# Optimization experiments

Measured on AMD Instinct MI355X. Metric: run time of the kernel, lower is better.

Reference implementation:

```python
import jax, jax.numpy as jnp
import numpy as np

TEMPERATURE = 0.07
UNIFORMITY_THRESHOLD = 0.1
SEPARATION_MARGIN = 2.0
W_SUPCON = 1.0
W_SEPARATION = 0.5
W_UNIFORMITY = 0.5
NUM_MASKS = 6


def setup_inputs() -> dict:
    key = jax.random.key(0)
    k1, k2, k3 = jax.random.split(key, 3)
    B, H, Wd, D = 16, 33, 33, 512
    emb = jax.random.normal(k1, (B, H, Wd, D), dtype=jnp.float32)
    emb = emb / jnp.linalg.norm(emb, axis=-1, keepdims=True)  # module expects normalized embeddings
    masks = jax.random.uniform(k2, (B, NUM_MASKS, H, Wd), dtype=jnp.float32)
    is_forged = jax.random.uniform(k3, (B,), dtype=jnp.float32)
    return {"embeddings": emb, "masks": masks, "is_forged": is_forged}


def _labels(masks):
    # masks: (M, H, W). Channel i writes label i+1 where mask>0.5 (if channel has any mass);
    # later channels overwrite earlier -> equivalent to max over active hits.
    active = masks.sum(axis=(1, 2)) > 0  # (M,)
    hit = (masks > 0.5) & active[:, None, None]
    ids = jnp.arange(1, masks.shape[0] + 1)[:, None, None]
    return jnp.max(jnp.where(hit, ids, 0), axis=0).reshape(-1)  # (H*W,)


def _per_image(emb, masks, forged):
    H, W, D = emb.shape
    feat = emb.reshape(-1, D)  # (N, D)
    N = feat.shape[0]
    labels = _labels(masks)  # (N,) in 0..M
    L = masks.shape[0] + 1  # possible labels 0..6
    onehot = (labels[:, None] == jnp.arange(L)[None, :]).astype(feat.dtype)  # (N, L)
    cnt = onehot.sum(axis=0)  # (L,)
    sums = onehot.T @ feat  # (L, D) per-label sums
    mean_l = sums / jnp.maximum(cnt, 1.0)[:, None]  # safe per-label centroids

    # ---- SupCon (PixelSupConLoss) ----
    logits = (feat @ feat.T) / TEMPERATURE  # (N, N)
    logits = logits - jax.lax.stop_gradient(logits.max(axis=1, keepdims=True))
    same = (labels[:, None] == labels[None, :]).astype(feat.dtype)
    logits_mask = 1.0 - jnp.eye(N, dtype=feat.dtype)
    pos = same * logits_mask
    exp_l = jnp.exp(logits) * logits_mask
    log_prob = logits - jnp.log(exp_l.sum(axis=1, keepdims=True) + 1e-6)
    pos_sum = pos.sum(axis=1)
    mean_lp = (pos * log_prob).sum(axis=1) / jnp.where(pos_sum == 0, 1.0, pos_sum)
    anchor_valid = (pos_sum > 0).astype(feat.dtype)
    n_anchor = anchor_valid.sum()
    supcon = (-mean_lp * anchor_valid).sum() / jnp.maximum(n_anchor, 1.0)
    supcon_valid = n_anchor > 0

    # ---- Inter-instance separation ----
    present = cnt > 0
    cn = (mean_l ** 2).sum(axis=1)  # (L,)
    sq = cn[:, None] + cn[None, :] - 2.0 * (mean_l @ mean_l.T)  # squared centroid dists
    tri = jnp.triu(jnp.ones((L, L), dtype=bool), k=1)
    pair_valid = tri & present[:, None] & present[None, :]
    d = jnp.sqrt(jnp.where(pair_valid, jnp.maximum(sq, 0.0), 1.0))
    terms = jnp.where(pair_valid, jax.nn.relu(SEPARATION_MARGIN - d), 0.0)
    n_pairs = pair_valid.sum().astype(feat.dtype)
    sep = terms.sum() / jnp.maximum(n_pairs, 1.0)
    sep_valid = present.sum() >= 2

    # ---- Uniformity ----
    rn2 = (feat ** 2).sum(axis=1)  # (N,)
    q_l = onehot.T @ rn2  # (L,) per-label sum of squared norms
    var_l = q_l / jnp.maximum(cnt, 1.0) - (mean_l ** 2).sum(axis=1)  # E||e||^2 - ||mean||^2
    lbl_valid = (cnt >= 2) & (var_l > UNIFORMITY_THRESHOLD)
    inst_loss = jnp.where(lbl_valid, var_l - UNIFORMITY_THRESHOLD, 0.0).sum()
    n_lbl = lbl_valid.sum().astype(feat.dtype)
    uni_forged = inst_loss / jnp.maximum(n_lbl, 1.0)
    uni_forged_valid = n_lbl > 0
    mean_all = feat.mean(axis=0)
    var_all = ((feat - mean_all) ** 2).sum(axis=1).mean()
    uni_unf = jnp.where(var_all > UNIFORMITY_THRESHOLD, var_all - UNIFORMITY_THRESHOLD, 0.0)
    uni_unf_valid = var_all > UNIFORMITY_THRESHOLD

    is_f = forged >= 0.5
    uni = jnp.where(is_f, uni_forged, uni_unf)
    uni_valid = jnp.where(is_f, uni_forged_valid, uni_unf_valid)
    return supcon, supcon_valid, sep, sep_valid, uni, uni_valid


def _agg(vals, valids):
    v = valids.astype(vals.dtype)
    n = v.sum()
    return jnp.where(n > 0, (vals * v).sum() / jnp.maximum(n, 1.0), 0.0)


def reference(embeddings, masks, is_forged):
    sc, scv, sp, spv, un, unv = jax.vmap(_per_image)(embeddings, masks, is_forged)
    supcon = _agg(sc, scv)
    separation = _agg(sp, spv)
    uniformity = _agg(un, unv)
    return W_SUPCON * supcon + W_SEPARATION * separation + W_UNIFORMITY * uniformity
```

## Files before the change

kernel.cpp:

```cpp
#include <hip/hip_runtime.h>
#include <math.h>

#define NPIX 1089
#define DIM 512
#define NIMG 16
#define NLBL 8
#define NMASK 6
#define INVT 14.2857142857142857f

#define NGRP 72
#define NROWPAD 1152
#define NT9 9



typedef short v8s __attribute__((ext_vector_type(8)));
typedef float v4f __attribute__((ext_vector_type(4)));

__device__ __forceinline__ float wave_reduce(float x) {
#pragma unroll
  for (int o = 32; o > 0; o >>= 1) x += __shfl_xor(x, o, 64);
  return x;
}
__device__ __forceinline__ unsigned bfbits(float x) {
  unsigned u = __float_as_uint(x);
  return (u + 0x7FFFu + ((u >> 16) & 1u)) >> 16;
}
__device__ __forceinline__ unsigned pk(float lo, float hi) {
  return bfbits(lo) | (bfbits(hi) << 16);
}

__global__ void k_labels(const float* __restrict__ masks, int* __restrict__ labels,
                         float* __restrict__ cnt) {
  int b = blockIdx.x, tid = threadIdx.x;
  int lane = tid & 63, w = tid >> 6;
  __shared__ float msum[NMASK];
  __shared__ float red[4][NLBL];
  if (tid < NMASK) msum[tid] = 0.f;
  __syncthreads();
  float acc[NMASK] = {0.f, 0.f, 0.f, 0.f, 0.f, 0.f};
  for (int p = tid; p < NPIX; p += 256) {
#pragma unroll
    for (int c = 0; c < NMASK; c++) acc[c] += masks[((size_t)b * NMASK + c) * NPIX + p];
  }
#pragma unroll
  for (int c = 0; c < NMASK; c++) {
    float v = wave_reduce(acc[c]);
    if (lane == 0) atomicAdd(&msum[c], v);
  }
  __syncthreads();
  float c8[NLBL] = {0.f, 0.f, 0.f, 0.f, 0.f, 0.f, 0.f, 0.f};
  for (int p = tid; p < NPIX; p += 256) {
    int lab = 0;
#pragma unroll
    for (int c = 0; c < NMASK; c++) {
      float mv = masks[((size_t)b * NMASK + c) * NPIX + p];
      if (mv > 0.5f && msum[c] > 0.f) lab = c + 1;
    }
    labels[b * NPIX + p] = lab;
#pragma unroll
    for (int l = 0; l < NLBL; l++) c8[l] += (lab == l) ? 1.f : 0.f;
  }
#pragma unroll
  for (int l = 0; l < NLBL; l++) c8[l] = wave_reduce(c8[l]);
  if (lane == 0) {
#pragma unroll
    for (int l = 0; l < NLBL; l++) red[w][l] = c8[l];
  }
  __syncthreads();
  if (tid < NLBL)
    cnt[b * NLBL + tid] = red[0][tid] + red[1][tid] + red[2][tid] + red[3][tid];
}

__global__ __launch_bounds__(512) void k_packsum(const float* __restrict__ emb,
                                                 const int* __restrict__ labels,
                                                 uint2* __restrict__ bfemb2,
                                                 float* __restrict__ sums9) {
  int b = blockIdx.y;
  int g9 = blockIdx.x >> 1, dh = blockIdx.x & 1;
  int tid = threadIdx.x, dd = tid & 63, w4 = tid >> 6;
  __shared__ int slab[128];
  __shared__ float4 red[8 * 8 * 64];
  if (tid < 128) {
    int r = g9 * 128 + tid;
    slab[tid] = (r < NPIX) ? labels[b * NPIX + r] : 7;
  }
  __syncthreads();
  float4 fa0 = {0,0,0,0}, fa1 = {0,0,0,0}, fa2 = {0,0,0,0}, fa3 = {0,0,0,0};
  float4 fa4 = {0,0,0,0}, fa5 = {0,0,0,0}, fa6 = {0,0,0,0}, fa7 = {0,0,0,0};
  int kc = dh * 8 + (dd >> 3), q = (dd >> 1) & 3, half = dd & 1;
#pragma unroll
  for (int k = 0; k < 16; k++) {
    int r = g9 * 128 + w4 + k * 8;
    bool v = r < NPIX;
    int rc = v ? r : (NPIX - 1);
    float4 x = ((const float4*)(emb + (size_t)(b * NPIX + rc) * DIM))[dh * 64 + dd];
    if (!v) x = make_float4(0.f, 0.f, 0.f, 0.f);
    uint2 o = make_uint2(pk(x.x, x.y), pk(x.z, x.w));
    bfemb2[((((size_t)(b * NGRP + (r >> 4)) * 16 + kc) * 64) + q * 16 + (r & 15)) * 2 + half] = o;
    int lab = __builtin_amdgcn_readfirstlane(slab[r - g9 * 128]);
    switch (lab) {
      case 0: fa0.x += x.x; fa0.y += x.y; fa0.z += x.z; fa0.w += x.w; break;
      case 1: fa1.x += x.x; fa1.y += x.y; fa1.z += x.z; fa1.w += x.w; break;
      case 2: fa2.x += x.x; fa2.y += x.y; fa2.z += x.z; fa2.w += x.w; break;
      case 3: fa3.x += x.x; fa3.y += x.y; fa3.z += x.z; fa3.w += x.w; break;
      case 4: fa4.x += x.x; fa4.y += x.y; fa4.z += x.z; fa4.w += x.w; break;
      case 5: fa5.x += x.x; fa5.y += x.y; fa5.z += x.z; fa5.w += x.w; break;
      case 6: fa6.x += x.x; fa6.y += x.y; fa6.z += x.z; fa6.w += x.w; break;
      default: fa7.x += x.x; fa7.y += x.y; fa7.z += x.z; fa7.w += x.w; break;
    }
  }
  red[(0 * 8 + w4) * 64 + dd] = fa0; red[(1 * 8 + w4) * 64 + dd] = fa1;
  red[(2 * 8 + w4) * 64 + dd] = fa2; red[(3 * 8 + w4) * 64 + dd] = fa3;
  red[(4 * 8 + w4) * 64 + dd] = fa4; red[(5 * 8 + w4) * 64 + dd] = fa5;
  red[(6 * 8 + w4) * 64 + dd] = fa6; red[(7 * 8 + w4) * 64 + dd] = fa7;
  __syncthreads();
  int l = tid >> 6, d2 = tid & 63;
  float4 s = {0,0,0,0};
#pragma unroll
  for (int ww = 0; ww < 8; ww++) {
    float4 t = red[(l * 8 + ww) * 64 + d2];
    s.x += t.x; s.y += t.y; s.z += t.z; s.w += t.w;
  }
  *(float4*)&sums9[(((size_t)(b * NT9 + g9) * NLBL + l) * DIM) + dh * 256 + d2 * 4] = s;
}

__global__ __launch_bounds__(256) void k_epass3(const uint4* __restrict__ bfemb4,
                                                float* __restrict__ E18) {
  int n = blockIdx.x;
  int img = ((n & 7) << 1) | ((n >> 3) & 1);
  int t = n >> 4;
  int it = 0, rem = t;
  while (rem >= NT9 - it) { rem -= NT9 - it; it++; }
  int jt = it + rem;
  int i0 = it * 128, j0 = jt * 128;
  bool diag = (it == jt);
  int tid = threadIdx.x, lane = tid & 63, w = tid >> 6;
  int wm = w >> 1, wn = w & 1;
  int quad = lane >> 4, l15 = lane & 15;

  size_t uA[4], uB[4];
#pragma unroll
  for (int f = 0; f < 4; f++) {
    uA[f] = ((size_t)(img * NGRP + it * 8 + wm * 4 + f) * 16) * 64 + lane;
    uB[f] = ((size_t)(img * NGRP + jt * 8 + wn * 4 + f) * 16) * 64 + lane;
  }

  v4f acc[4][4];
#pragma unroll
  for (int mf = 0; mf < 4; mf++)
#pragma unroll
    for (int nf = 0; nf < 4; nf++) acc[mf][nf] = (v4f){0.f, 0.f, 0.f, 0.f};

  v8s a0[4], b0[4], a1[4], b1[4];
#define LOADG(kc, AR, BR)                                               \
  {                                                                     \
    _Pragma("unroll") for (int f = 0; f < 4; f++)                       \
        AR[f] = *(const v8s*)(bfemb4 + uA[f] + (kc) * 64);              \
    _Pragma("unroll") for (int f = 0; f < 4; f++)                       \
        BR[f] = *(const v8s*)(bfemb4 + uB[f] + (kc) * 64);              \
  }
#define MFMAG(AR, BR)                                                   \
  {                                                                     \
    _Pragma("unroll") for (int mf = 0; mf < 4; mf++)                    \
        _Pragma("unroll") for (int nf = 0; nf < 4; nf++)                \
            acc[mf][nf] = __builtin_amdgcn_mfma_f32_16x16x32_bf16(      \
                AR[mf], BR[nf], acc[mf][nf], 0, 0, 0);                  \
  }

  LOADG(0, a0, b0);
#pragma unroll
  for (int kc = 0; kc < 16; kc += 2) {
    if (kc + 1 < 16) LOADG(kc + 1, a1, b1);
    MFMAG(a0, b0);
    if (kc + 2 < 16) LOADG(kc + 2, a0, b0);
    MFMAG(a1, b1);
  }
#undef LOADG
#undef MFMAG

  float* Erow = E18 + ((size_t)img * 18 + jt * 2 + wn) * NROWPAD;
  float* Ecol = E18 + ((size_t)img * 18 + it * 2 + wm) * NROWPAD;
  float scol[4] = {0.f, 0.f, 0.f, 0.f};
#pragma unroll
  for (int mf = 0; mf < 4; mf++) {
#pragma unroll
    for (int rr = 0; rr < 4; rr++) {
      int i = i0 + wm * 64 + mf * 16 + quad * 4 + rr;
      float srow = 0.f;
#pragma unroll
      for (int nf = 0; nf < 4; nf++) {
        int j = j0 + wn * 64 + nf * 16 + l15;
        float e = __expf((acc[mf][nf][rr] - 1.f) * INVT);
        bool ok = (j < NPIX) && (!diag || (i != j && i < NPIX));
        e = ok ? e : 0.f;
        srow += e;
        scol[nf] += e;
      }
      srow += __shfl_xor(srow, 1); srow += __shfl_xor(srow, 2);
      srow += __shfl_xor(srow, 4); srow += __shfl_xor(srow, 8);
      if (l15 == 0) Erow[i] = srow;
    }
  }
  if (!diag) {
#pragma unroll
    for (int nf = 0; nf < 4; nf++) {
      float s = scol[nf];
      s += __shfl_xor(s, 16); s += __shfl_xor(s, 32);
      int j = j0 + wn * 64 + nf * 16 + l15;
      if (quad == 0) Ecol[j] = s;
    }
  }
}

__global__ void k_img(const float* __restrict__ sums9, const int* __restrict__ labels,
                      const float* __restrict__ cnt, const float* __restrict__ E18,
                      const float* __restrict__ is_forged, float* __restrict__ per_img) {
  int b = blockIdx.x, tid = threadIdx.x;
  int wave = tid >> 6, lane = tid & 63;
  __shared__ float ssum[NLBL * DIM];
  __shared__ float sCnt[NLBL], sR[NLBL][NLBL];
  __shared__ float sLog, sNA;
  if (tid < NLBL) sCnt[tid] = cnt[b * NLBL + tid];
  if (tid == 0) { sLog = 0.f; sNA = 0.f; }
  for (int o = tid; o < NLBL * DIM; o += 256) {
    float s = 0.f;
#pragma unroll
    for (int g = 0; g < NT9; g++) s += sums9[((size_t)(b * NT9 + g) * NLBL * DIM) + o];
    ssum[o] = s;
  }
  __syncthreads();
  float ll = 0.f, na = 0.f;
  for (int p = tid; p < NPIX; p += 256) {
    int lab = labels[b * NPIX + p];
    if (sCnt[lab] >= 1.5f) {
      float e = 0.f;
#pragma unroll
      for (int s = 0; s < 18; s++) e += E18[((size_t)b * 18 + s) * NROWPAD + p];
      ll += logf(e + 1e-6f);
      na += 1.f;
    }
  }
  ll = wave_reduce(ll); na = wave_reduce(na);
  if (lane == 0) { atomicAdd(&sLog, ll); atomicAdd(&sNA, na); }
  for (int t = wave; t < 36; t += 4) {
    int a = 0, tt = t;
    while (tt >= NLBL - a) { tt -= NLBL - a; a++; }
    int bb = a + tt;
    float d0 = 0.f;
    for (int k = lane; k < DIM; k += 64) d0 += ssum[a * DIM + k] * ssum[bb * DIM + k];
    d0 = wave_reduce(d0);
    if (lane == 0) sR[a][bb] = d0;
  }
  __syncthreads();
  if (tid == 0) {
    float spos = 0.f;
    for (int l = 0; l < NLBL; l++) {
      float c = sCnt[l];
      if (c >= 1.5f) spos += (sR[l][l] - c) * INVT / (c - 1.f) - c * INVT;
    }
    float nA = sNA;
    float sc = nA > 0.f ? (sLog - spos) / nA : 0.f;
    float scv = nA > 0.f ? 1.f : 0.f;
    float inv[NLBL]; int present[NLBL]; int nPres = 0;
    for (int l = 0; l < NLBL; l++) {
      present[l] = sCnt[l] > 0.f;
      nPres += present[l];
      inv[l] = 1.f / fmaxf(sCnt[l], 1.f);
    }
    float sepsum = 0.f; int npairs = 0;
    for (int a = 0; a < NLBL; a++)
      for (int c = a + 1; c < NLBL; c++)
        if (present[a] && present[c]) {
          float sq_ = sR[a][a] * inv[a] * inv[a] + sR[c][c] * inv[c] * inv[c]
                    - 2.f * sR[a][c] * inv[a] * inv[c];
          float dd = sqrtf(fmaxf(sq_, 0.f));
          sepsum += fmaxf(2.f - dd, 0.f);
          npairs++;
        }
    float sep = npairs > 0 ? sepsum / (float)npairs : 0.f;
    float sepv = nPres >= 2 ? 1.f : 0.f;
    float inst = 0.f; int nlbl = 0;
    for (int l = 0; l < NLBL; l++) {
      float var = 1.f - sR[l][l] * inv[l] * inv[l];
      if (sCnt[l] >= 2.f && var > 0.1f) { inst += var - 0.1f; nlbl++; }
    }
    float unif = nlbl > 0 ? inst / (float)nlbl : 0.f;
    float unifv = nlbl > 0 ? 1.f : 0.f;
    float tot2 = 0.f;
    for (int a = 0; a < NLBL; a++) {
      tot2 += sR[a][a];
      for (int c = a + 1; c < NLBL; c++) tot2 += 2.f * sR[a][c];
    }
    float Nf = (float)NPIX;
    float var_all = 1.f - tot2 / (Nf * Nf);
    float uniu = var_all > 0.1f ? var_all - 0.1f : 0.f;
    float uniuv = var_all > 0.1f ? 1.f : 0.f;
    bool isf = is_forged[b] >= 0.5f;
    per_img[b * 6 + 0] = sc;
    per_img[b * 6 + 1] = scv;
    per_img[b * 6 + 2] = sep;
    per_img[b * 6 + 3] = sepv;
    per_img[b * 6 + 4] = isf ? unif : uniu;
    per_img[b * 6 + 5] = isf ? unifv : uniuv;
  }
}

__global__ void k_final(const float* __restrict__ per_img, float* __restrict__ out) {
  if (threadIdx.x == 0) {
    float accv[3] = {0.f, 0.f, 0.f}, accn[3] = {0.f, 0.f, 0.f};
    for (int b = 0; b < NIMG; b++)
      for (int m = 0; m < 3; m++) {
        float v = per_img[b * 6 + m * 2], val = per_img[b * 6 + m * 2 + 1];
        accv[m] += v * val; accn[m] += val;
      }
    float sc = accn[0] > 0.f ? accv[0] / accn[0] : 0.f;
    float sep = accn[1] > 0.f ? accv[1] / accn[1] : 0.f;
    float uni = accn[2] > 0.f ? accv[2] / accn[2] : 0.f;
    out[0] = 1.0f * sc + 0.5f * sep + 0.5f * uni;
  }
}

extern "C" void kernel_launch(void* const* d_in, const int* in_sizes, int n_in,
                              void* d_out, int out_size, void* d_ws, size_t ws_size,
                              hipStream_t stream) {
  const float* emb = (const float*)d_in[0];
  const float* masks = (const float*)d_in[1];
  const float* isf = (const float*)d_in[2];
  float* out = (float*)d_out;
  char* ws = (char*)d_ws;
  size_t off = 0;
  uint4* bfemb4 = (uint4*)(ws + off);
  off += (size_t)NIMG * NGRP * 16 * 64 * 16;
  float* E18 = (float*)(ws + off);    off += sizeof(float) * NIMG * 18 * NROWPAD;
  float* sums9 = (float*)(ws + off);  off += sizeof(float) * NIMG * NT9 * NLBL * DIM;
  int* labels = (int*)(ws + off);     off += sizeof(int) * NIMG * NPIX;
  float* cnt = (float*)(ws + off);    off += sizeof(float) * NIMG * NLBL;
  float* per_img = (float*)(ws + off); off += sizeof(float) * NIMG * 6;

  k_labels<<<NIMG, 256, 0, stream>>>(masks, labels, cnt);
  k_packsum<<<dim3(18, NIMG), 512, 0, stream>>>(emb, labels, (uint2*)bfemb4, sums9);
  k_epass3<<<45 * NIMG, 256, 0, stream>>>(bfemb4, E18);
  k_img<<<NIMG, 256, 0, stream>>>(sums9, labels, cnt, E18, isf, per_img);
  k_final<<<1, 64, 0, stream>>>(per_img, out);
}
```

Baseline: 140.2 us.

## Fuse label computation into pack and image kernels, drop label and final launches

Removes the separate label kernel by recomputing mask sums and labels inside the pack-sum kernel and again inside the per-image kernel. The final aggregation kernel is folded into the per-image kernel through an atomic ticket counter that is reset inside the pack kernel. The row/column exp sums of each tile are combined in shared memory before being written, which halves the E buffer from 18 to 9 slices per image. The aim is fewer launches and less global traffic. The cost is redundant mask reads in every pack block and reliance on a counter reset earlier in the same stream.

```diff
diff --git a/kernel.cpp b/kernel.cpp
--- a/kernel.cpp
+++ b/kernel.cpp
@@ -13,7 +13,6 @@
 #define NT9 9
 
 
-
 typedef short v8s __attribute__((ext_vector_type(8)));
 typedef float v4f __attribute__((ext_vector_type(4)));
 
@@ -30,60 +29,45 @@
   return bfbits(lo) | (bfbits(hi) << 16);
 }
 
-__global__ void k_labels(const float* __restrict__ masks, int* __restrict__ labels,
-                         float* __restrict__ cnt) {
-  int b = blockIdx.x, tid = threadIdx.x;
-  int lane = tid & 63, w = tid >> 6;
-  __shared__ float msum[NMASK];
-  __shared__ float red[4][NLBL];
-  if (tid < NMASK) msum[tid] = 0.f;
-  __syncthreads();
-  float acc[NMASK] = {0.f, 0.f, 0.f, 0.f, 0.f, 0.f};
-  for (int p = tid; p < NPIX; p += 256) {
-#pragma unroll
-    for (int c = 0; c < NMASK; c++) acc[c] += masks[((size_t)b * NMASK + c) * NPIX + p];
-  }
-#pragma unroll
-  for (int c = 0; c < NMASK; c++) {
-    float v = wave_reduce(acc[c]);
-    if (lane == 0) atomicAdd(&msum[c], v);
-  }
-  __syncthreads();
-  float c8[NLBL] = {0.f, 0.f, 0.f, 0.f, 0.f, 0.f, 0.f, 0.f};
-  for (int p = tid; p < NPIX; p += 256) {
-    int lab = 0;
-#pragma unroll
-    for (int c = 0; c < NMASK; c++) {
-      float mv = masks[((size_t)b * NMASK + c) * NPIX + p];
-      if (mv > 0.5f && msum[c] > 0.f) lab = c + 1;
-    }
-    labels[b * NPIX + p] = lab;
-#pragma unroll
-    for (int l = 0; l < NLBL; l++) c8[l] += (lab == l) ? 1.f : 0.f;
-  }
-#pragma unroll
-  for (int l = 0; l < NLBL; l++) c8[l] = wave_reduce(c8[l]);
-  if (lane == 0) {
-#pragma unroll
-    for (int l = 0; l < NLBL; l++) red[w][l] = c8[l];
-  }
-  __syncthreads();
-  if (tid < NLBL)
-    cnt[b * NLBL + tid] = red[0][tid] + red[1][tid] + red[2][tid] + red[3][tid];
-}
-
 __global__ __launch_bounds__(512) void k_packsum(const float* __restrict__ emb,
-                                                 const int* __restrict__ labels,
+                                                 const float* __restrict__ masks,
                                                  uint2* __restrict__ bfemb2,
-                                                 float* __restrict__ sums9) {
+                                                 float* __restrict__ sums9,
+                                                 unsigned* __restrict__ counter) {
   int b = blockIdx.y;
   int g9 = blockIdx.x >> 1, dh = blockIdx.x & 1;
-  int tid = threadIdx.x, dd = tid & 63, w4 = tid >> 6;
+  int tid = threadIdx.x, dd = tid & 63, w4 = tid >> 6, lane = tid & 63;
+  __shared__ float msum[NMASK];
   __shared__ int slab[128];
   __shared__ float4 red[8 * 8 * 64];
+  if (tid < NMASK) msum[tid] = 0.f;
+  if (tid == 0 && blockIdx.x == 0 && b == 0) *counter = 0u;
+  __syncthreads();
+  {
+    float am[NMASK] = {0.f, 0.f, 0.f, 0.f, 0.f, 0.f};
+    for (int p = tid; p < NPIX; p += 512) {
+#pragma unroll
+      for (int c = 0; c < NMASK; c++) am[c] += masks[((size_t)b * NMASK + c) * NPIX + p];
+    }
+#pragma unroll
+    for (int c = 0; c < NMASK; c++) {
+      float v = wave_reduce(am[c]);
+      if (lane == 0) atomicAdd(&msum[c], v);
+    }
+  }
+  __syncthreads();
   if (tid < 128) {
     int r = g9 * 128 + tid;
-    slab[tid] = (r < NPIX) ? labels[b * NPIX + r] : 7;
+    int lab = 7;
+    if (r < NPIX) {
+      lab = 0;
+#pragma unroll
+      for (int c = 0; c < NMASK; c++) {
+        float mv = masks[((size_t)b * NMASK + c) * NPIX + r];
+        if (mv > 0.5f && msum[c] > 0.f) lab = c + 1;
+      }
+    }
+    slab[tid] = lab;
   }
   __syncthreads();
   float4 fa0 = {0,0,0,0}, fa1 = {0,0,0,0}, fa2 = {0,0,0,0}, fa3 = {0,0,0,0};
@@ -126,7 +110,7 @@
 }
 
 __global__ __launch_bounds__(256) void k_epass3(const uint4* __restrict__ bfemb4,
-                                                float* __restrict__ E18) {
+                                                float* __restrict__ E9) {
   int n = blockIdx.x;
   int img = ((n & 7) << 1) | ((n >> 3) & 1);
   int t = n >> 4;
@@ -138,6 +122,8 @@
   int tid = threadIdx.x, lane = tid & 63, w = tid >> 6;
   int wm = w >> 1, wn = w & 1;
   int quad = lane >> 4, l15 = lane & 15;
+  __shared__ float Ered[2][128];
+  __shared__ float Ecol[2][128];
 
   size_t uA[4], uB[4];
 #pragma unroll
@@ -179,8 +165,6 @@
 #undef LOADG
 #undef MFMAG
 
-  float* Erow = E18 + ((size_t)img * 18 + jt * 2 + wn) * NROWPAD;
-  float* Ecol = E18 + ((size_t)img * 18 + it * 2 + wm) * NROWPAD;
   float scol[4] = {0.f, 0.f, 0.f, 0.f};
 #pragma unroll
   for (int mf = 0; mf < 4; mf++) {
@@ -199,7 +183,7 @@
       }
       srow += __shfl_xor(srow, 1); srow += __shfl_xor(srow, 2);
       srow += __shfl_xor(srow, 4); srow += __shfl_xor(srow, 8);
-      if (l15 == 0) Erow[i] = srow;
+      if (l15 == 0) Ered[wn][wm * 64 + mf * 16 + quad * 4 + rr] = srow;
     }
   }
   if (!diag) {
@@ -207,22 +191,68 @@
     for (int nf = 0; nf < 4; nf++) {
       float s = scol[nf];
       s += __shfl_xor(s, 16); s += __shfl_xor(s, 32);
-      int j = j0 + wn * 64 + nf * 16 + l15;
-      if (quad == 0) Ecol[j] = s;
-    }
-  }
-}
-
-__global__ void k_img(const float* __restrict__ sums9, const int* __restrict__ labels,
-                      const float* __restrict__ cnt, const float* __restrict__ E18,
-                      const float* __restrict__ is_forged, float* __restrict__ per_img) {
+      if (quad == 0) Ecol[wm][wn * 64 + nf * 16 + l15] = s;
+    }
+  }
+  __syncthreads();
+  if (tid < 128) {
+    E9[((size_t)img * NT9 + jt) * NROWPAD + i0 + tid] = Ered[0][tid] + Ered[1][tid];
+    if (!diag)
+      E9[((size_t)img * NT9 + it) * NROWPAD + j0 + tid] = Ecol[0][tid] + Ecol[1][tid];
+  }
+}
+
+__global__ void k_imgfinal(const float* __restrict__ masks, const float* __restrict__ sums9,
+                           const float* __restrict__ E9, const float* __restrict__ is_forged,
+                           unsigned* __restrict__ counter, float* __restrict__ per_img,
+                           float* __restrict__ out) {
   int b = blockIdx.x, tid = threadIdx.x;
   int wave = tid >> 6, lane = tid & 63;
+  __shared__ float msum[NMASK];
+  __shared__ int slab[NPIX];
   __shared__ float ssum[NLBL * DIM];
   __shared__ float sCnt[NLBL], sR[NLBL][NLBL];
+  __shared__ float red4[4][NLBL];
   __shared__ float sLog, sNA;
-  if (tid < NLBL) sCnt[tid] = cnt[b * NLBL + tid];
+  if (tid < NMASK) msum[tid] = 0.f;
   if (tid == 0) { sLog = 0.f; sNA = 0.f; }
+  __syncthreads();
+  {
+    float am[NMASK] = {0.f, 0.f, 0.f, 0.f, 0.f, 0.f};
+    for (int p = tid; p < NPIX; p += 256) {
+#pragma unroll
+      for (int c = 0; c < NMASK; c++) am[c] += masks[((size_t)b * NMASK + c) * NPIX + p];
+    }
+#pragma unroll
+    for (int c = 0; c < NMASK; c++) {
+      float v = wave_reduce(am[c]);
+      if (lane == 0) atomicAdd(&msum[c], v);
+    }
+  }
+  __syncthreads();
+  {
+    float c8[NLBL] = {0.f, 0.f, 0.f, 0.f, 0.f, 0.f, 0.f, 0.f};
+    for (int p = tid; p < NPIX; p += 256) {
+      int lab = 0;
+#pragma unroll
+      for (int c = 0; c < NMASK; c++) {
+        float mv = masks[((size_t)b * NMASK + c) * NPIX + p];
+        if (mv > 0.5f && msum[c] > 0.f) lab = c + 1;
+      }
+      slab[p] = lab;
+#pragma unroll
+      for (int l = 0; l < NLBL; l++) c8[l] += (lab == l) ? 1.f : 0.f;
+    }
+#pragma unroll
+    for (int l = 0; l < NLBL; l++) c8[l] = wave_reduce(c8[l]);
+    if (lane == 0) {
+#pragma unroll
+      for (int l = 0; l < NLBL; l++) red4[wave][l] = c8[l];
+    }
+  }
+  __syncthreads();
+  if (tid < NLBL)
+    sCnt[tid] = red4[0][tid] + red4[1][tid] + red4[2][tid] + red4[3][tid];
   for (int o = tid; o < NLBL * DIM; o += 256) {
     float s = 0.f;
 #pragma unroll
@@ -232,11 +262,11 @@
   __syncthreads();
   float ll = 0.f, na = 0.f;
   for (int p = tid; p < NPIX; p += 256) {
-    int lab = labels[b * NPIX + p];
+    int lab = slab[p];
     if (sCnt[lab] >= 1.5f) {
       float e = 0.f;
 #pragma unroll
-      for (int s = 0; s < 18; s++) e += E18[((size_t)b * 18 + s) * NROWPAD + p];
+      for (int s = 0; s < NT9; s++) e += E9[((size_t)b * NT9 + s) * NROWPAD + p];
       ll += logf(e + 1e-6f);
       na += 1.f;
     }
@@ -303,21 +333,21 @@
     per_img[b * 6 + 3] = sepv;
     per_img[b * 6 + 4] = isf ? unif : uniu;
     per_img[b * 6 + 5] = isf ? unifv : uniuv;
-  }
-}
-
-__global__ void k_final(const float* __restrict__ per_img, float* __restrict__ out) {
-  if (threadIdx.x == 0) {
-    float accv[3] = {0.f, 0.f, 0.f}, accn[3] = {0.f, 0.f, 0.f};
-    for (int b = 0; b < NIMG; b++)
-      for (int m = 0; m < 3; m++) {
-        float v = per_img[b * 6 + m * 2], val = per_img[b * 6 + m * 2 + 1];
-        accv[m] += v * val; accn[m] += val;
-      }
-    float sc = accn[0] > 0.f ? accv[0] / accn[0] : 0.f;
-    float sep = accn[1] > 0.f ? accv[1] / accn[1] : 0.f;
-    float uni = accn[2] > 0.f ? accv[2] / accn[2] : 0.f;
-    out[0] = 1.0f * sc + 0.5f * sep + 0.5f * uni;
+    __threadfence();
+    unsigned tk = atomicAdd(counter, 1u);
+    if (tk == NIMG - 1) {
+      __threadfence();
+      float accv[3] = {0.f, 0.f, 0.f}, accn[3] = {0.f, 0.f, 0.f};
+      for (int bb = 0; bb < NIMG; bb++)
+        for (int m = 0; m < 3; m++) {
+          float v = per_img[bb * 6 + m * 2], val = per_img[bb * 6 + m * 2 + 1];
+          accv[m] += v * val; accn[m] += val;
+        }
+      float scA = accn[0] > 0.f ? accv[0] / accn[0] : 0.f;
+      float sepA = accn[1] > 0.f ? accv[1] / accn[1] : 0.f;
+      float uniA = accn[2] > 0.f ? accv[2] / accn[2] : 0.f;
+      out[0] = 1.0f * scA + 0.5f * sepA + 0.5f * uniA;
+    }
   }
 }
 
@@ -332,15 +362,13 @@
   size_t off = 0;
   uint4* bfemb4 = (uint4*)(ws + off);
   off += (size_t)NIMG * NGRP * 16 * 64 * 16;
-  float* E18 = (float*)(ws + off);    off += sizeof(float) * NIMG * 18 * NROWPAD;
+  float* E9 = (float*)(ws + off);     off += sizeof(float) * NIMG * NT9 * NROWPAD;
   float* sums9 = (float*)(ws + off);  off += sizeof(float) * NIMG * NT9 * NLBL * DIM;
-  int* labels = (int*)(ws + off);     off += sizeof(int) * NIMG * NPIX;
-  float* cnt = (float*)(ws + off);    off += sizeof(float) * NIMG * NLBL;
   float* per_img = (float*)(ws + off); off += sizeof(float) * NIMG * 6;
-
-  k_labels<<<NIMG, 256, 0, stream>>>(masks, labels, cnt);
-  k_packsum<<<dim3(18, NIMG), 512, 0, stream>>>(emb, labels, (uint2*)bfemb4, sums9);
-  k_epass3<<<45 * NIMG, 256, 0, stream>>>(bfemb4, E18);
-  k_img<<<NIMG, 256, 0, stream>>>(sums9, labels, cnt, E18, isf, per_img);
-  k_final<<<1, 64, 0, stream>>>(per_img, out);
-}
+  off = (off + 127) & ~(size_t)127;
+  unsigned* counter = (unsigned*)(ws + off); off += 128;
+
+  k_packsum<<<dim3(18, NIMG), 512, 0, stream>>>(emb, masks, (uint2*)bfemb4, sums9, counter);
+  k_epass3<<<45 * NIMG, 256, 0, stream>>>(bfemb4, E9);
+  k_imgfinal<<<NIMG, 256, 0, stream>>>(masks, sums9, E9, isf, counter, per_img, out);
+}
```

Result: no change. 142.7 us (+1.8%).

## Fuse final reduction into per-image kernel and halve row-sum partials via LDS

Applied to the files above, without the earlier changes.

The per-tile row and column exp-sums are now combined across the two wave halves in shared memory before being written, which halves the partial-sum buffer (9 slices instead of 18) and the reads in the per-image kernel. The per-image kernel runs with 512 threads, uses the fast log intrinsic, and does the final cross-image aggregation itself: the last block to finish, found through an atomic counter reset in the label kernel, computes the output. This removes one kernel launch and some global traffic. In exchange the epass kernel gains a block barrier, and the last-block pattern relies on threadfence ordering.

```diff
diff --git a/kernel.cpp b/kernel.cpp
--- a/kernel.cpp
+++ b/kernel.cpp
@@ -13,7 +13,6 @@
 #define NT9 9
 
 
-
 typedef short v8s __attribute__((ext_vector_type(8)));
 typedef float v4f __attribute__((ext_vector_type(4)));
 
@@ -31,12 +30,13 @@
 }
 
 __global__ void k_labels(const float* __restrict__ masks, int* __restrict__ labels,
-                         float* __restrict__ cnt) {
+                         float* __restrict__ cnt, unsigned* __restrict__ counter) {
   int b = blockIdx.x, tid = threadIdx.x;
   int lane = tid & 63, w = tid >> 6;
   __shared__ float msum[NMASK];
   __shared__ float red[4][NLBL];
   if (tid < NMASK) msum[tid] = 0.f;
+  if (b == 0 && tid == 0) *counter = 0u;
   __syncthreads();
   float acc[NMASK] = {0.f, 0.f, 0.f, 0.f, 0.f, 0.f};
   for (int p = tid; p < NPIX; p += 256) {
@@ -126,7 +126,7 @@
 }
 
 __global__ __launch_bounds__(256) void k_epass3(const uint4* __restrict__ bfemb4,
-                                                float* __restrict__ E18) {
+                                                float* __restrict__ E9) {
   int n = blockIdx.x;
   int img = ((n & 7) << 1) | ((n >> 3) & 1);
   int t = n >> 4;
@@ -138,6 +138,8 @@
   int tid = threadIdx.x, lane = tid & 63, w = tid >> 6;
   int wm = w >> 1, wn = w & 1;
   int quad = lane >> 4, l15 = lane & 15;
+  __shared__ float Ered[2][128];
+  __shared__ float Ecol[2][128];
 
   size_t uA[4], uB[4];
 #pragma unroll
@@ -179,8 +181,6 @@
 #undef LOADG
 #undef MFMAG
 
-  float* Erow = E18 + ((size_t)img * 18 + jt * 2 + wn) * NROWPAD;
-  float* Ecol = E18 + ((size_t)img * 18 + it * 2 + wm) * NROWPAD;
   float scol[4] = {0.f, 0.f, 0.f, 0.f};
 #pragma unroll
   for (int mf = 0; mf < 4; mf++) {
@@ -199,7 +199,7 @@
       }
       srow += __shfl_xor(srow, 1); srow += __shfl_xor(srow, 2);
       srow += __shfl_xor(srow, 4); srow += __shfl_xor(srow, 8);
-      if (l15 == 0) Erow[i] = srow;
+      if (l15 == 0) Ered[wn][wm * 64 + mf * 16 + quad * 4 + rr] = srow;
     }
   }
   if (!diag) {
@@ -207,15 +207,25 @@
     for (int nf = 0; nf < 4; nf++) {
       float s = scol[nf];
       s += __shfl_xor(s, 16); s += __shfl_xor(s, 32);
-      int j = j0 + wn * 64 + nf * 16 + l15;
-      if (quad == 0) Ecol[j] = s;
-    }
-  }
-}
-
-__global__ void k_img(const float* __restrict__ sums9, const int* __restrict__ labels,
-                      const float* __restrict__ cnt, const float* __restrict__ E18,
-                      const float* __restrict__ is_forged, float* __restrict__ per_img) {
+      if (quad == 0) Ecol[wm][wn * 64 + nf * 16 + l15] = s;
+    }
+  }
+  __syncthreads();
+  if (tid < 128) {
+    E9[((size_t)img * NT9 + jt) * NROWPAD + i0 + tid] = Ered[0][tid] + Ered[1][tid];
+    if (!diag)
+      E9[((size_t)img * NT9 + it) * NROWPAD + j0 + tid] = Ecol[0][tid] + Ecol[1][tid];
+  }
+}
+
+__global__ __launch_bounds__(512) void k_imgfinal(const float* __restrict__ sums9,
+                                                  const int* __restrict__ labels,
+                                                  const float* __restrict__ cnt,
+                                                  const float* __restrict__ E9,
+                                                  const float* __restrict__ is_forged,
+                                                  unsigned* __restrict__ counter,
+                                                  float* __restrict__ per_img,
+                                                  float* __restrict__ out) {
   int b = blockIdx.x, tid = threadIdx.x;
   int wave = tid >> 6, lane = tid & 63;
   __shared__ float ssum[NLBL * DIM];
@@ -223,7 +233,7 @@
   __shared__ float sLog, sNA;
   if (tid < NLBL) sCnt[tid] = cnt[b * NLBL + tid];
   if (tid == 0) { sLog = 0.f; sNA = 0.f; }
-  for (int o = tid; o < NLBL * DIM; o += 256) {
+  for (int o = tid; o < NLBL * DIM; o += 512) {
     float s = 0.f;
 #pragma unroll
     for (int g = 0; g < NT9; g++) s += sums9[((size_t)(b * NT9 + g) * NLBL * DIM) + o];
@@ -231,19 +241,19 @@
   }
   __syncthreads();
   float ll = 0.f, na = 0.f;
-  for (int p = tid; p < NPIX; p += 256) {
+  for (int p = tid; p < NPIX; p += 512) {
     int lab = labels[b * NPIX + p];
     if (sCnt[lab] >= 1.5f) {
       float e = 0.f;
 #pragma unroll
-      for (int s = 0; s < 18; s++) e += E18[((size_t)b * 18 + s) * NROWPAD + p];
-      ll += logf(e + 1e-6f);
+      for (int s = 0; s < NT9; s++) e += E9[((size_t)b * NT9 + s) * NROWPAD + p];
+      ll += __logf(e + 1e-6f);
       na += 1.f;
     }
   }
   ll = wave_reduce(ll); na = wave_reduce(na);
   if (lane == 0) { atomicAdd(&sLog, ll); atomicAdd(&sNA, na); }
-  for (int t = wave; t < 36; t += 4) {
+  for (int t = wave; t < 36; t += 8) {
     int a = 0, tt = t;
     while (tt >= NLBL - a) { tt -= NLBL - a; a++; }
     int bb = a + tt;
@@ -303,21 +313,21 @@
     per_img[b * 6 + 3] = sepv;
     per_img[b * 6 + 4] = isf ? unif : uniu;
     per_img[b * 6 + 5] = isf ? unifv : uniuv;
-  }
-}
-
-__global__ void k_final(const float* __restrict__ per_img, float* __restrict__ out) {
-  if (threadIdx.x == 0) {
-    float accv[3] = {0.f, 0.f, 0.f}, accn[3] = {0.f, 0.f, 0.f};
-    for (int b = 0; b < NIMG; b++)
-      for (int m = 0; m < 3; m++) {
-        float v = per_img[b * 6 + m * 2], val = per_img[b * 6 + m * 2 + 1];
-        accv[m] += v * val; accn[m] += val;
-      }
-    float sc = accn[0] > 0.f ? accv[0] / accn[0] : 0.f;
-    float sep = accn[1] > 0.f ? accv[1] / accn[1] : 0.f;
-    float uni = accn[2] > 0.f ? accv[2] / accn[2] : 0.f;
-    out[0] = 1.0f * sc + 0.5f * sep + 0.5f * uni;
+    __threadfence();
+    unsigned tk = atomicAdd(counter, 1u);
+    if (tk == NIMG - 1) {
+      __threadfence();
+      float accv[3] = {0.f, 0.f, 0.f}, accn[3] = {0.f, 0.f, 0.f};
+      for (int bb = 0; bb < NIMG; bb++)
+        for (int m = 0; m < 3; m++) {
+          float v = per_img[bb * 6 + m * 2], val = per_img[bb * 6 + m * 2 + 1];
+          accv[m] += v * val; accn[m] += val;
+        }
+      float scA = accn[0] > 0.f ? accv[0] / accn[0] : 0.f;
+      float sepA = accn[1] > 0.f ? accv[1] / accn[1] : 0.f;
+      float uniA = accn[2] > 0.f ? accv[2] / accn[2] : 0.f;
+      out[0] = 1.0f * scA + 0.5f * sepA + 0.5f * uniA;
+    }
   }
 }
 
@@ -332,15 +342,16 @@
   size_t off = 0;
   uint4* bfemb4 = (uint4*)(ws + off);
   off += (size_t)NIMG * NGRP * 16 * 64 * 16;
-  float* E18 = (float*)(ws + off);    off += sizeof(float) * NIMG * 18 * NROWPAD;
+  float* E9 = (float*)(ws + off);     off += sizeof(float) * NIMG * NT9 * NROWPAD;
   float* sums9 = (float*)(ws + off);  off += sizeof(float) * NIMG * NT9 * NLBL * DIM;
   int* labels = (int*)(ws + off);     off += sizeof(int) * NIMG * NPIX;
   float* cnt = (float*)(ws + off);    off += sizeof(float) * NIMG * NLBL;
   float* per_img = (float*)(ws + off); off += sizeof(float) * NIMG * 6;
-
-  k_labels<<<NIMG, 256, 0, stream>>>(masks, labels, cnt);
+  off = (off + 127) & ~(size_t)127;
+  unsigned* counter = (unsigned*)(ws + off); off += 128;
+
+  k_labels<<<NIMG, 256, 0, stream>>>(masks, labels, cnt, counter);
   k_packsum<<<dim3(18, NIMG), 512, 0, stream>>>(emb, labels, (uint2*)bfemb4, sums9);
-  k_epass3<<<45 * NIMG, 256, 0, stream>>>(bfemb4, E18);
-  k_img<<<NIMG, 256, 0, stream>>>(sums9, labels, cnt, E18, isf, per_img);
-  k_final<<<1, 64, 0, stream>>>(per_img, out);
-}
+  k_epass3<<<45 * NIMG, 256, 0, stream>>>(bfemb4, E9);
+  k_imgfinal<<<NIMG, 512, 0, stream>>>(sums9, labels, cnt, E9, isf, counter, per_img, out);
+}
```

New measurement: 136.4 us. -2.7%, faster.
